# Kernel tuning notes

Measured on AMD Instinct MI355X. Metric: run time of the kernel, lower is better.

Reference implementation:

```python
import jax, jax.numpy as jnp
import numpy as np

B, N, E, IDX = 4, 200000, 128, 2048


def setup_inputs() -> dict:
    key = jax.random.key(0)
    ks = jax.random.split(key, 6)
    x = jax.random.normal(ks[0], (B, N, E), dtype=jnp.float32)
    mask = jax.random.randint(ks[1], (B, N), 0, 2).astype(jnp.int32)
    index = jax.random.randint(ks[2], (B, N), 0, IDX).astype(jnp.int32)
    W = jax.random.normal(ks[3], (E, E), dtype=jnp.float32) * 0.05
    b = jax.random.normal(ks[4], (E,), dtype=jnp.float32) * 0.05
    context = jax.random.normal(ks[5], (E,), dtype=jnp.float32)
    return {"x": x, "W": W, "b": b, "context": context, "mask": mask, "index": index}


def _segment_attend(scores, idx, xb):
    # scores: [N], idx: [N] int, xb: [N, E]
    m = jax.ops.segment_max(scores, idx, num_segments=IDX)  # [IDX]
    m = jnp.where(jnp.isfinite(m), m, 0.0)  # empty segments -> -inf guard
    e = jnp.exp(scores - m[idx])
    ssum = jax.ops.segment_sum(e, idx, num_segments=IDX)  # [IDX]
    w = e / ssum[idx]  # segment softmax weights, [N]
    out = jax.ops.segment_sum(xb * w[:, None], idx, num_segments=IDX)  # [IDX, E]
    return out, w


def reference(x, W, b, context, mask, index):
    norm = jnp.sqrt(jnp.asarray(E, dtype=x.dtype))
    hidden = jnp.tanh(jnp.einsum('bne,fe->bnf', x, W) + b)  # Linear(E,E) + tanh
    importance = jnp.einsum('bne,e->bn', hidden, context) / norm
    importance = jnp.where(mask == 0, jnp.asarray(-1e9, dtype=x.dtype), importance)
    out, attn = jax.vmap(_segment_attend)(importance, index, x)
    return out, attn
```

## Files before the change

### kernel.cpp

```cpp
#include <hip/hip_runtime.h>
#include <hip/hip_bf16.h>
#include <math.h>

#define B_    4
#define N_    200000
#define E_    128
#define IDX_  2048
#define TT    (B_*N_)
#define INV_NORM 0.08838834764831845f
#define CAP   512
#define RCAP  8
#define WPAD  136

typedef __attribute__((ext_vector_type(8))) short bf16x8;
typedef __attribute__((ext_vector_type(4))) float f32x4;

__device__ __forceinline__ unsigned short f2bf(float f) {
    unsigned int u = __float_as_uint(f);
    unsigned int r = (u + 0x7fffu + ((u >> 16) & 1u)) >> 16;
    return (unsigned short)r;
}

__global__ __launch_bounds__(256) void score_kernel(
    const float* __restrict__ x, const float* __restrict__ W,
    const float* __restrict__ bias, const float* __restrict__ ctx,
    const int* __restrict__ mask, const int* __restrict__ index,
    float* __restrict__ scores, int* __restrict__ counts)
{
    __shared__ unsigned short Wb[E_ * WPAD];

    const int tid = threadIdx.x;

    for (int i = tid; i < E_ * E_ / 4; i += 256) {
        int f = i >> 5, kb = (i & 31) * 4;
        float4 v = ((const float4*)W)[i];
        ushort4 o;
        o.x = f2bf(v.x); o.y = f2bf(v.y); o.z = f2bf(v.z); o.w = f2bf(v.w);
        *(ushort4*)&Wb[f * WPAD + kb] = o;
    }
    __syncthreads();

    const int lane = tid & 63;
    const int col  = lane & 15;
    const int q    = lane >> 4;
    const int wave = tid >> 6;

    float ctx_r[8], bias2[8], csum = 0.f;
#pragma unroll
    for (int n = 0; n < 8; n++) {
        ctx_r[n] = ctx[n * 16 + col];
        bias2[n] = 2.f * bias[n * 16 + col];
        csum += ctx_r[n];
    }
    const float csum_n = csum * INV_NORM;

    bf16x8 Bf[8][4];
#pragma unroll
    for (int n = 0; n < 8; n++)
#pragma unroll
        for (int kt = 0; kt < 4; kt++)
            Bf[n][kt] = *(const bf16x8*)&Wb[(n * 16 + col) * WPAD + kt * 32 + q * 8];

    for (long base0 = (long)blockIdx.x * 64; base0 < TT; base0 += (long)gridDim.x * 64) {
        const long tbase = base0 + wave * 16;
        const float* xrow = x + (tbase + col) * (long)E_;

        bf16x8 Af[4];
#pragma unroll
        for (int kt = 0; kt < 4; kt++) {
            float4 u = ((const float4*)xrow)[kt * 8 + q * 2];
            float4 v = ((const float4*)xrow)[kt * 8 + q * 2 + 1];
            union { bf16x8 vec; __hip_bfloat162 h[4]; } a;
            a.h[0] = __float22bfloat162_rn(make_float2(u.x, u.y));
            a.h[1] = __float22bfloat162_rn(make_float2(u.z, u.w));
            a.h[2] = __float22bfloat162_rn(make_float2(v.x, v.y));
            a.h[3] = __float22bfloat162_rn(make_float2(v.z, v.w));
            Af[kt] = a.vec;
        }

        f32x4 acc[8];
#pragma unroll
        for (int n = 0; n < 8; n++) acc[n] = (f32x4){0.f, 0.f, 0.f, 0.f};

#pragma unroll
        for (int kt = 0; kt < 4; kt++)
#pragma unroll
            for (int n = 0; n < 8; n++)
                acc[n] = __builtin_amdgcn_mfma_f32_16x16x32_bf16(Af[kt], Bf[n][kt], acc[n], 0, 0, 0);

        float pr[4];
#pragma unroll
        for (int r = 0; r < 4; r++) {
            float psum = 0.f;
#pragma unroll
            for (int n = 0; n < 8; n++) {
                float t = fmaf(acc[n][r], 2.f, bias2[n]);
                float rc = __builtin_amdgcn_rcpf(1.f + __expf(t));
                psum = fmaf(ctx_r[n], rc, psum);
            }
            float p = fmaf(-2.f * INV_NORM, psum, csum_n);
#pragma unroll
            for (int o = 1; o < 16; o <<= 1) p += __shfl_xor(p, o);
            pr[r] = p;
        }
        if (col == 0) {
            int4 mv = ((const int4*)(mask + tbase))[q];
            float4 s;
            s.x = mv.x ? pr[0] : -1e9f;
            s.y = mv.y ? pr[1] : -1e9f;
            s.z = mv.z ? pr[2] : -1e9f;
            s.w = mv.w ? pr[3] : -1e9f;
            ((float4*)(scores + tbase))[q] = s;

            int4 iv = ((const int4*)(index + tbase))[q];
            int* cb = counts + (int)(tbase / N_) * IDX_;
            atomicAdd(&cb[iv.x], 1);
            atomicAdd(&cb[iv.y], 1);
            atomicAdd(&cb[iv.z], 1);
            atomicAdd(&cb[iv.w], 1);
        }
    }
}

__global__ __launch_bounds__(1024) void scan_kernel(
    const int* __restrict__ counts, int* __restrict__ offsets, int* __restrict__ cursor)
{
    __shared__ int sums[1024];
    int tid = threadIdx.x;
    int c[8], loc[8], s = 0;
#pragma unroll
    for (int j = 0; j < 8; j++) { c[j] = counts[tid * 8 + j]; loc[j] = s; s += c[j]; }
    sums[tid] = s;
    __syncthreads();
    for (int off = 1; off < 1024; off <<= 1) {
        int v = (tid >= off) ? sums[tid - off] : 0;
        __syncthreads();
        if (tid >= off) sums[tid] += v;
        __syncthreads();
    }
    int base = (tid > 0) ? sums[tid - 1] : 0;
#pragma unroll
    for (int j = 0; j < 8; j++) {
        int o = base + loc[j];
        offsets[tid * 8 + j] = o;
        cursor[tid * 8 + j]  = o;
    }
}

__global__ __launch_bounds__(256) void scatter_kernel(
    const int* __restrict__ index, const float* __restrict__ scores,
    int* __restrict__ cursor, int2* __restrict__ tokenlist)
{
    for (int tok = blockIdx.x * blockDim.x + threadIdx.x; tok < TT;
         tok += gridDim.x * blockDim.x) {
        int seg = index[tok];
        float s = scores[tok];
        int b   = tok / N_;
        int pos = atomicAdd(&cursor[b * IDX_ + seg], 1);
        tokenlist[pos] = make_int2(tok, __float_as_int(s));
    }
}

__global__ __launch_bounds__(256) void attend_kernel(
    const float* __restrict__ x, const int* __restrict__ counts,
    const int* __restrict__ offsets, const int2* __restrict__ tokenlist,
    float* __restrict__ attn , float* __restrict__ out)
{
    const int wave = threadIdx.x >> 6;
    const int lane = threadIdx.x & 63;
    const int key  = blockIdx.x * 4 + wave;
    const int cnt  = counts[key];
    const int off  = offsets[key];
    const float2* __restrict__ x2 = (const float2*)x;
    float2* out2 = (float2*)(out + (size_t)key * E_);

    __shared__ int2 pair[4][CAP];

    if (cnt == 0) { out2[lane] = make_float2(0.f, 0.f); return; }

    if (cnt <= CAP) {
        int   tk[RCAP];
        float sc[RCAP], ev[RCAP];
        float m = -INFINITY;
#pragma unroll
        for (int u = 0; u < RCAP; u++) {
            int j = lane + u * 64;
            if (j < cnt) {
                int2 p = tokenlist[off + j];
                tk[u] = p.x;
                sc[u] = __int_as_float(p.y);
                m = fmaxf(m, sc[u]);
            }
        }
#pragma unroll
        for (int o = 32; o; o >>= 1) m = fmaxf(m, __shfl_xor(m, o));

        float sum = 0.f;
#pragma unroll
        for (int u = 0; u < RCAP; u++) {
            int j = lane + u * 64;
            if (j < cnt) { ev[u] = __expf(sc[u] - m); sum += ev[u]; }
        }
#pragma unroll
        for (int o = 32; o; o >>= 1) sum += __shfl_xor(sum, o);
        const float inv = 1.f / sum;

#pragma unroll
        for (int u = 0; u < RCAP; u++) {
            int j = lane + u * 64;
            if (j < cnt) {
                float w = ev[u] * inv;
                attn[tk[u]] = w;
                pair[wave][j] = make_int2(tk[u], __float_as_int(w));
            }
        }

        float2 acc = make_float2(0.f, 0.f);
        int j = 0;
        for (; j + 3 < cnt; j += 4) {
            int2 p0 = pair[wave][j];
            int2 p1 = pair[wave][j + 1];
            int2 p2 = pair[wave][j + 2];
            int2 p3 = pair[wave][j + 3];
            float2 a0 = x2[(size_t)p0.x * 64 + lane];
            float2 a1 = x2[(size_t)p1.x * 64 + lane];
            float2 a2 = x2[(size_t)p2.x * 64 + lane];
            float2 a3 = x2[(size_t)p3.x * 64 + lane];
            float w0 = __int_as_float(p0.y), w1 = __int_as_float(p1.y);
            float w2 = __int_as_float(p2.y), w3 = __int_as_float(p3.y);
            acc.x = fmaf(w0, a0.x, acc.x); acc.y = fmaf(w0, a0.y, acc.y);
            acc.x = fmaf(w1, a1.x, acc.x); acc.y = fmaf(w1, a1.y, acc.y);
            acc.x = fmaf(w2, a2.x, acc.x); acc.y = fmaf(w2, a2.y, acc.y);
            acc.x = fmaf(w3, a3.x, acc.x); acc.y = fmaf(w3, a3.y, acc.y);
        }
        for (; j < cnt; j++) {
            int2  p = pair[wave][j];
            float2 a = x2[(size_t)p.x * 64 + lane];
            float w = __int_as_float(p.y);
            acc.x = fmaf(w, a.x, acc.x); acc.y = fmaf(w, a.y, acc.y);
        }
        out2[lane] = acc;
    } else {
        float m = -INFINITY;
        for (int j = lane; j < cnt; j += 64)
            m = fmaxf(m, __int_as_float(tokenlist[off + j].y));
#pragma unroll
        for (int o = 32; o; o >>= 1) m = fmaxf(m, __shfl_xor(m, o));

        float sum = 0.f;
        for (int j = lane; j < cnt; j += 64)
            sum += __expf(__int_as_float(tokenlist[off + j].y) - m);
#pragma unroll
        for (int o = 32; o; o >>= 1) sum += __shfl_xor(sum, o);
        const float inv = 1.f / sum;

        float2 acc = make_float2(0.f, 0.f);
        for (int j0 = 0; j0 < cnt; j0 += 64) {
            int t = 0; float w = 0.f;
            if (j0 + lane < cnt) {
                int2 p = tokenlist[off + j0 + lane];
                t = p.x;
                w = __expf(__int_as_float(p.y) - m) * inv;
                attn[t] = w;
            }
            int lim = min(64, cnt - j0);
            for (int jj = 0; jj < lim; jj++) {
                int   tb = __shfl(t, jj);
                float wb = __shfl(w, jj);
                float2 a = x2[(size_t)tb * 64 + lane];
                acc.x = fmaf(wb, a.x, acc.x);
                acc.y = fmaf(wb, a.y, acc.y);
            }
        }
        out2[lane] = acc;
    }
}

extern "C" void kernel_launch(void* const* d_in, const int* in_sizes, int n_in,
                              void* d_out, int out_size, void* d_ws, size_t ws_size,
                              hipStream_t stream)
{
    const float* x    = (const float*)d_in[0];
    const float* W    = (const float*)d_in[1];
    const float* bias = (const float*)d_in[2];
    const float* ctx  = (const float*)d_in[3];
    const int*   mask = (const int*)d_in[4];
    const int*   index= (const int*)d_in[5];

    float* out  = (float*)d_out;
    float* attn = out + (size_t)B_ * IDX_ * E_;

    int* counts    = (int*)d_ws;
    int* offsets   = counts  + B_ * IDX_;
    int* cursor    = offsets + B_ * IDX_;
    int2* tokenlist = (int2*)(cursor + B_ * IDX_);

    hipMemsetAsync(counts, 0, B_ * IDX_ * sizeof(int), stream);
    score_kernel  <<<2048, 256, 0, stream>>>(x, W, bias, ctx, mask, index, attn, counts);
    scan_kernel   <<<1, 1024, 0, stream>>>(counts, offsets, cursor);
    scatter_kernel<<<1024, 256, 0, stream>>>(index, attn, cursor, tokenlist);
    attend_kernel <<<B_ * IDX_ / 4, 256, 0, stream>>>(x, counts, offsets, tokenlist, attn, out);
}
```

Measured before the change: 735.3 us.

## Drop masked tokens before scoring and build compact per-segment score lists

Reorders the pipeline so the histogram, scan and scatter steps run first and include only unmasked tokens. A position map lets the score kernel write each score straight into a compact per-segment array. The score kernel skips loading x rows for masked tokens, and the attend kernel no longer gathers masked rows, which cuts HBM traffic on the large x tensor. Masked tokens get attention weight zero directly. This differs from the reference only when every token in a segment is masked, where the reference gives uniform weights. It adds an extra pass over mask and index plus a posmap buffer.

```diff
diff --git a/kernel.cpp b/kernel.cpp
--- a/kernel.cpp
+++ b/kernel.cpp
@@ -21,103 +21,16 @@
     return (unsigned short)r;
 }
 
-__global__ __launch_bounds__(256) void score_kernel(
-    const float* __restrict__ x, const float* __restrict__ W,
-    const float* __restrict__ bias, const float* __restrict__ ctx,
-    const int* __restrict__ mask, const int* __restrict__ index,
-    float* __restrict__ scores, int* __restrict__ counts)
-{
-    __shared__ unsigned short Wb[E_ * WPAD];
-
-    const int tid = threadIdx.x;
-
-    for (int i = tid; i < E_ * E_ / 4; i += 256) {
-        int f = i >> 5, kb = (i & 31) * 4;
-        float4 v = ((const float4*)W)[i];
-        ushort4 o;
-        o.x = f2bf(v.x); o.y = f2bf(v.y); o.z = f2bf(v.z); o.w = f2bf(v.w);
-        *(ushort4*)&Wb[f * WPAD + kb] = o;
-    }
-    __syncthreads();
-
-    const int lane = tid & 63;
-    const int col  = lane & 15;
-    const int q    = lane >> 4;
-    const int wave = tid >> 6;
-
-    float ctx_r[8], bias2[8], csum = 0.f;
-#pragma unroll
-    for (int n = 0; n < 8; n++) {
-        ctx_r[n] = ctx[n * 16 + col];
-        bias2[n] = 2.f * bias[n * 16 + col];
-        csum += ctx_r[n];
-    }
-    const float csum_n = csum * INV_NORM;
-
-    bf16x8 Bf[8][4];
-#pragma unroll
-    for (int n = 0; n < 8; n++)
-#pragma unroll
-        for (int kt = 0; kt < 4; kt++)
-            Bf[n][kt] = *(const bf16x8*)&Wb[(n * 16 + col) * WPAD + kt * 32 + q * 8];
-
-    for (long base0 = (long)blockIdx.x * 64; base0 < TT; base0 += (long)gridDim.x * 64) {
-        const long tbase = base0 + wave * 16;
-        const float* xrow = x + (tbase + col) * (long)E_;
-
-        bf16x8 Af[4];
-#pragma unroll
-        for (int kt = 0; kt < 4; kt++) {
-            float4 u = ((const float4*)xrow)[kt * 8 + q * 2];
-            float4 v = ((const float4*)xrow)[kt * 8 + q * 2 + 1];
-            union { bf16x8 vec; __hip_bfloat162 h[4]; } a;
-            a.h[0] = __float22bfloat162_rn(make_float2(u.x, u.y));
-            a.h[1] = __float22bfloat162_rn(make_float2(u.z, u.w));
-            a.h[2] = __float22bfloat162_rn(make_float2(v.x, v.y));
-            a.h[3] = __float22bfloat162_rn(make_float2(v.z, v.w));
-            Af[kt] = a.vec;
-        }
-
-        f32x4 acc[8];
-#pragma unroll
-        for (int n = 0; n < 8; n++) acc[n] = (f32x4){0.f, 0.f, 0.f, 0.f};
-
-#pragma unroll
-        for (int kt = 0; kt < 4; kt++)
-#pragma unroll
-            for (int n = 0; n < 8; n++)
-                acc[n] = __builtin_amdgcn_mfma_f32_16x16x32_bf16(Af[kt], Bf[n][kt], acc[n], 0, 0, 0);
-
-        float pr[4];
-#pragma unroll
-        for (int r = 0; r < 4; r++) {
-            float psum = 0.f;
-#pragma unroll
-            for (int n = 0; n < 8; n++) {
-                float t = fmaf(acc[n][r], 2.f, bias2[n]);
-                float rc = __builtin_amdgcn_rcpf(1.f + __expf(t));
-                psum = fmaf(ctx_r[n], rc, psum);
-            }
-            float p = fmaf(-2.f * INV_NORM, psum, csum_n);
-#pragma unroll
-            for (int o = 1; o < 16; o <<= 1) p += __shfl_xor(p, o);
-            pr[r] = p;
-        }
-        if (col == 0) {
-            int4 mv = ((const int4*)(mask + tbase))[q];
-            float4 s;
-            s.x = mv.x ? pr[0] : -1e9f;
-            s.y = mv.y ? pr[1] : -1e9f;
-            s.z = mv.z ? pr[2] : -1e9f;
-            s.w = mv.w ? pr[3] : -1e9f;
-            ((float4*)(scores + tbase))[q] = s;
-
-            int4 iv = ((const int4*)(index + tbase))[q];
-            int* cb = counts + (int)(tbase / N_) * IDX_;
-            atomicAdd(&cb[iv.x], 1);
-            atomicAdd(&cb[iv.y], 1);
-            atomicAdd(&cb[iv.z], 1);
-            atomicAdd(&cb[iv.w], 1);
+__global__ __launch_bounds__(256) void hist_kernel(
+    const int* __restrict__ index, const int* __restrict__ mask,
+    int* __restrict__ counts, float* __restrict__ attn)
+{
+    for (int tok = blockIdx.x * blockDim.x + threadIdx.x; tok < TT;
+         tok += gridDim.x * blockDim.x) {
+        if (mask[tok]) {
+            atomicAdd(&counts[(tok / N_) * IDX_ + index[tok]], 1);
+        } else {
+            attn[tok] = 0.f;
         }
     }
 }
@@ -148,22 +61,124 @@
 }
 
 __global__ __launch_bounds__(256) void scatter_kernel(
-    const int* __restrict__ index, const float* __restrict__ scores,
-    int* __restrict__ cursor, int2* __restrict__ tokenlist)
+    const int* __restrict__ index, const int* __restrict__ mask,
+    int* __restrict__ cursor, int* __restrict__ toklist, int* __restrict__ posmap)
 {
     for (int tok = blockIdx.x * blockDim.x + threadIdx.x; tok < TT;
          tok += gridDim.x * blockDim.x) {
-        int seg = index[tok];
-        float s = scores[tok];
-        int b   = tok / N_;
-        int pos = atomicAdd(&cursor[b * IDX_ + seg], 1);
-        tokenlist[pos] = make_int2(tok, __float_as_int(s));
+        int pos = 0;
+        if (mask[tok]) {
+            pos = atomicAdd(&cursor[(tok / N_) * IDX_ + index[tok]], 1);
+            toklist[pos] = tok;
+        }
+        posmap[tok] = pos;
+    }
+}
+
+__global__ __launch_bounds__(256) void score_kernel(
+    const float* __restrict__ x, const float* __restrict__ W,
+    const float* __restrict__ bias, const float* __restrict__ ctx,
+    const int* __restrict__ mask, const int* __restrict__ posmap,
+    float* __restrict__ pscore)
+{
+    __shared__ unsigned short Wb[E_ * WPAD];
+
+    const int tid = threadIdx.x;
+
+    for (int i = tid; i < E_ * E_ / 4; i += 256) {
+        int f = i >> 5, kb = (i & 31) * 4;
+        float4 v = ((const float4*)W)[i];
+        ushort4 o;
+        o.x = f2bf(v.x); o.y = f2bf(v.y); o.z = f2bf(v.z); o.w = f2bf(v.w);
+        *(ushort4*)&Wb[f * WPAD + kb] = o;
+    }
+    __syncthreads();
+
+    const int lane = tid & 63;
+    const int col  = lane & 15;
+    const int q    = lane >> 4;
+    const int wave = tid >> 6;
+
+    float ctx_r[8], bias2[8], csum = 0.f;
+#pragma unroll
+    for (int n = 0; n < 8; n++) {
+        ctx_r[n] = ctx[n * 16 + col];
+        bias2[n] = 2.f * bias[n * 16 + col];
+        csum += ctx_r[n];
+    }
+    const float csum_n = csum * INV_NORM;
+
+    bf16x8 Bf[8][4];
+#pragma unroll
+    for (int n = 0; n < 8; n++)
+#pragma unroll
+        for (int kt = 0; kt < 4; kt++)
+            Bf[n][kt] = *(const bf16x8*)&Wb[(n * 16 + col) * WPAD + kt * 32 + q * 8];
+
+    for (long base0 = (long)blockIdx.x * 64; base0 < TT; base0 += (long)gridDim.x * 64) {
+        const long tbase = base0 + wave * 16;
+        const float* xrow = x + (tbase + col) * (long)E_;
+
+        const int mrow = mask[tbase + col];
+
+        bf16x8 Af[4];
+#pragma unroll
+        for (int kt = 0; kt < 4; kt++)
+            Af[kt] = (bf16x8){0, 0, 0, 0, 0, 0, 0, 0};
+        if (mrow) {
+#pragma unroll
+            for (int kt = 0; kt < 4; kt++) {
+                float4 u = ((const float4*)xrow)[kt * 8 + q * 2];
+                float4 v = ((const float4*)xrow)[kt * 8 + q * 2 + 1];
+                union { bf16x8 vec; __hip_bfloat162 h[4]; } a;
+                a.h[0] = __float22bfloat162_rn(make_float2(u.x, u.y));
+                a.h[1] = __float22bfloat162_rn(make_float2(u.z, u.w));
+                a.h[2] = __float22bfloat162_rn(make_float2(v.x, v.y));
+                a.h[3] = __float22bfloat162_rn(make_float2(v.z, v.w));
+                Af[kt] = a.vec;
+            }
+        }
+
+        f32x4 acc[8];
+#pragma unroll
+        for (int n = 0; n < 8; n++) acc[n] = (f32x4){0.f, 0.f, 0.f, 0.f};
+
+#pragma unroll
+        for (int kt = 0; kt < 4; kt++)
+#pragma unroll
+            for (int n = 0; n < 8; n++)
+                acc[n] = __builtin_amdgcn_mfma_f32_16x16x32_bf16(Af[kt], Bf[n][kt], acc[n], 0, 0, 0);
+
+        float pr[4];
+#pragma unroll
+        for (int r = 0; r < 4; r++) {
+            float psum = 0.f;
+#pragma unroll
+            for (int n = 0; n < 8; n++) {
+                float t = fmaf(acc[n][r], 2.f, bias2[n]);
+                float rc = __builtin_amdgcn_rcpf(1.f + __expf(t));
+                psum = fmaf(ctx_r[n], rc, psum);
+            }
+            float p = fmaf(-2.f * INV_NORM, psum, csum_n);
+#pragma unroll
+            for (int o = 1; o < 16; o <<= 1) p += __shfl_xor(p, o);
+            pr[r] = p;
+        }
+        if (col == 0) {
+            int4 mv = ((const int4*)(mask + tbase))[q];
+            int4 pm = ((const int4*)(posmap + tbase))[q];
+            if (mv.x) pscore[pm.x] = pr[0];
+            if (mv.y) pscore[pm.y] = pr[1];
+            if (mv.z) pscore[pm.z] = pr[2];
+            if (mv.w) pscore[pm.w] = pr[3];
+        }
     }
 }
 
 __global__ __launch_bounds__(256) void attend_kernel(
     const float* __restrict__ x, const int* __restrict__ counts,
-    const int* __restrict__ offsets, const int2* __restrict__ tokenlist,
+    const int* __restrict__ offsets, const int* __restrict__ toklist,
+    const float* __restrict__ pscore,
     float* __restrict__ attn , float* __restrict__ out)
 {
     const int wave = threadIdx.x >> 6;
@@ -186,9 +201,8 @@
         for (int u = 0; u < RCAP; u++) {
             int j = lane + u * 64;
             if (j < cnt) {
-                int2 p = tokenlist[off + j];
-                tk[u] = p.x;
-                sc[u] = __int_as_float(p.y);
+                tk[u] = toklist[off + j];
+                sc[u] = pscore[off + j];
                 m = fmaxf(m, sc[u]);
             }
         }
@@ -243,13 +257,13 @@
     } else {
         float m = -INFINITY;
         for (int j = lane; j < cnt; j += 64)
-            m = fmaxf(m, __int_as_float(tokenlist[off + j].y));
+            m = fmaxf(m, pscore[off + j]);
 #pragma unroll
         for (int o = 32; o; o >>= 1) m = fmaxf(m, __shfl_xor(m, o));
 
         float sum = 0.f;
         for (int j = lane; j < cnt; j += 64)
-            sum += __expf(__int_as_float(tokenlist[off + j].y) - m);
+            sum += __expf(pscore[off + j] - m);
 #pragma unroll
         for (int o = 32; o; o >>= 1) sum += __shfl_xor(sum, o);
         const float inv = 1.f / sum;
@@ -258,9 +272,8 @@
         for (int j0 = 0; j0 < cnt; j0 += 64) {
             int t = 0; float w = 0.f;
             if (j0 + lane < cnt) {
-                int2 p = tokenlist[off + j0 + lane];
-                t = p.x;
-                w = __expf(__int_as_float(p.y) - m) * inv;
+                t = toklist[off + j0 + lane];
+                w = __expf(pscore[off + j0 + lane] - m) * inv;
                 attn[t] = w;
             }
             int lim = min(64, cnt - j0);
@@ -290,14 +303,17 @@
     float* out  = (float*)d_out;
     float* attn = out + (size_t)B_ * IDX_ * E_;
 
-    int* counts    = (int*)d_ws;
-    int* offsets   = counts  + B_ * IDX_;
-    int* cursor    = offsets + B_ * IDX_;
-    int2* tokenlist = (int2*)(cursor + B_ * IDX_);
+    int*   counts  = (int*)d_ws;
+    int*   offsets = counts  + B_ * IDX_;
+    int*   cursor  = offsets + B_ * IDX_;
+    int*   toklist = cursor  + B_ * IDX_;
+    int*   posmap  = toklist + TT;
+    float* pscore  = (float*)(posmap + TT);
 
     hipMemsetAsync(counts, 0, B_ * IDX_ * sizeof(int), stream);
-    score_kernel  <<<2048, 256, 0, stream>>>(x, W, bias, ctx, mask, index, attn, counts);
+    hist_kernel   <<<2048, 256, 0, stream>>>(index, mask, counts, attn);
     scan_kernel   <<<1, 1024, 0, stream>>>(counts, offsets, cursor);
-    scatter_kernel<<<1024, 256, 0, stream>>>(index, attn, cursor, tokenlist);
-    attend_kernel <<<B_ * IDX_ / 4, 256, 0, stream>>>(x, counts, offsets, tokenlist, attn, out);
-}
+    scatter_kernel<<<2048, 256, 0, stream>>>(index, mask, cursor, toklist, posmap);
+    score_kernel  <<<2048, 256, 0, stream>>>(x, W, bias, ctx, mask, posmap, pscore);
+    attend_kernel <<<B_ * IDX_ / 4, 256, 0, stream>>>(x, counts, offsets, toklist, pscore, attn, out);
+}
```

Result: faster. 666.8 us (-9.3%).
